# Kernel tuning notes

Measured on AMD Instinct MI355X. Metric: run time of the kernel, lower is better.

## Reference

```python
import jax, jax.numpy as jnp
import numpy as np

SMALL_CONST = 1e-8
K = 128
N = 512 * 512  # pixels


def setup_inputs() -> dict:
    key = jax.random.key(0)
    ks = jax.random.split(key, 6)
    pos = jax.random.uniform(ks[0], (N, 2), jnp.float32, 0.0, 512.0)      # pixel coords
    mu = jax.random.uniform(ks[1], (K, 2), jnp.float32, 0.0, 512.0)       # gaussian centers
    alpha = jax.random.uniform(ks[2], (K,), jnp.float32)                   # opacities in [0,1]
    color = jax.random.uniform(ks[3], (K, 3), jnp.float32, 0.0, 255.0)     # RGB in [0,255]
    scales = 10.0 + jax.random.uniform(ks[4], (K, 2), jnp.float32) * 20.0  # anisotropic scales
    thetas = jax.random.uniform(ks[5], (K,), jnp.float32, -np.pi, np.pi)   # rotations
    return dict(pos=pos, mu=mu, alpha=alpha, color=color, scales=scales, thetas=thetas)


def _forward(pos, mu, alpha, color, scales, thetas):
    # Parameter clamps done at the top of the torch forward
    alpha = jnp.clip(alpha, 0.0, 1.0)
    color = jnp.clip(color, 0.0, 255.0)
    scales = jnp.clip(scales, 0.1, None)

    # Precompute all K inverse covariances: sigma_inv = R diag(1/s^2) R^T  -> [K,2,2]
    c, s = jnp.cos(thetas), jnp.sin(thetas)
    R = jnp.stack([jnp.stack([c, -s], -1), jnp.stack([s, c], -1)], -2)  # [K,2,2]
    inv2 = 1.0 / scales ** 2                                            # [K,2]
    sigma_inv = jnp.einsum('kti,ki,kji->ktj', R, inv2, R)               # [K,2,2]

    n = pos.shape[0]
    pc0 = jnp.zeros((n, 3), pos.dtype)
    pa0 = jnp.zeros((n, 1), pos.dtype)

    def step(carry, g):
        pc, pa = carry
        mu_k, si_k, a_k, col_k = g
        diff = pos - mu_k                                          # [N,2]
        expo = -0.5 * jnp.einsum('ni,ij,nj->n', diff, si_k, diff)  # [N]
        alpha_k = (a_k * jnp.exp(expo))[:, None]                   # [N,1]
        new_alpha = pa + alpha_k * (1.0 - pa)
        pc = (pc * pa + col_k * alpha_k * (1.0 - pa)) / (new_alpha + SMALL_CONST)
        pc = jnp.clip(pc, 0.0, 255.0)
        pa = jnp.clip(new_alpha, 0.0, 1.0)
        return (pc, pa), None

    (pc, pa), _ = jax.lax.scan(jax.checkpoint(step), (pc0, pa0),
                               (mu, sigma_inv, alpha, color))
    # include_opc=True path: append alpha channel scaled to [0,255]
    return jnp.concatenate([pc, pa * 255.0], axis=-1)  # [N,4]


def reference(pos, mu, alpha, color, scales, thetas):
    return _forward(pos, mu, alpha, color, scales, thetas)
```

## Files before the change

kernel.cpp:

```cpp
#include <hip/hip_runtime.h>
#include <math.h>

#define KG 128

__global__ __launch_bounds__(256) void splat_fwd(
    const float* __restrict__ pos,
    const float* __restrict__ mu,
    const float* __restrict__ alpha,
    const float* __restrict__ color,
    const float* __restrict__ scales,
    const float* __restrict__ thetas,
    float* __restrict__ out,
    int n)
{
    __shared__ float4 sP0[KG];
    __shared__ float4 sP1[KG];
    __shared__ float  sP2[KG];

    const int tid = threadIdx.x;
    if (tid < KG) {
        const int k = tid;
        const float mx = mu[2 * k];
        const float my = mu[2 * k + 1];
        const float al = fminf(fmaxf(alpha[k], 0.0f), 1.0f);
        const float cr = fminf(fmaxf(color[3 * k + 0], 0.0f), 255.0f);
        const float cg = fminf(fmaxf(color[3 * k + 1], 0.0f), 255.0f);
        const float cb = fminf(fmaxf(color[3 * k + 2], 0.0f), 255.0f);
        const float sx = fmaxf(scales[2 * k + 0], 0.1f);
        const float sy = fmaxf(scales[2 * k + 1], 0.1f);
        const float th = thetas[k];
        const float c = cosf(th);
        const float s = sinf(th);
        const float i0 = 1.0f / (sx * sx);
        const float i1 = 1.0f / (sy * sy);
        const float a  = c * c * i0 + s * s * i1;
        const float b  = c * s * (i0 - i1);
        const float cc = s * s * i0 + c * c * i1;
        const float f = -0.5f * 1.4426950408889634f;
        sP0[k] = make_float4(mx, my, a * f, 2.0f * b * f);
        sP1[k] = make_float4(cc * f, al, cr, cg);
        sP2[k] = cb;
    }
    __syncthreads();

    const int i = blockIdx.x * blockDim.x + tid;
    if (i >= n) return;

    const float2 p = reinterpret_cast<const float2*>(pos)[i];

    float pa = 0.0f;
    float pcr = 0.0f, pcg = 0.0f, pcb = 0.0f;

#pragma unroll 4
    for (int k = 0; k < KG; ++k) {
        const float4 q0 = sP0[k];
        const float4 q1 = sP1[k];
        const float  q2 = sP2[k];
        const float dx = p.x - q0.x;
        const float dy = p.y - q0.y;
        const float e = q0.z * (dx * dx) + q0.w * (dx * dy) + q1.x * (dy * dy);
        const float w = q1.y * __builtin_amdgcn_exp2f(e);

        const float omp = 1.0f - pa;
        const float t1  = w * omp;
        const float na  = pa + t1;
        const float r   = __builtin_amdgcn_rcpf(na + 1e-8f);

        pcr = fminf(fmaxf((pcr * pa + q1.z * t1) * r, 0.0f), 255.0f);
        pcg = fminf(fmaxf((pcg * pa + q1.w * t1) * r, 0.0f), 255.0f);
        pcb = fminf(fmaxf((pcb * pa + q2  * t1) * r, 0.0f), 255.0f);
        pa  = fminf(na, 1.0f);
    }

    float4 o;
    o.x = pcr;
    o.y = pcg;
    o.z = pcb;
    o.w = pa * 255.0f;
    reinterpret_cast<float4*>(out)[i] = o;
}

extern "C" void kernel_launch(void* const* d_in, const int* in_sizes, int n_in,
                              void* d_out, int out_size, void* d_ws, size_t ws_size,
                              hipStream_t stream) {
    const float* pos    = (const float*)d_in[0];
    const float* mu     = (const float*)d_in[1];
    const float* alpha  = (const float*)d_in[2];
    const float* color  = (const float*)d_in[3];
    const float* scales = (const float*)d_in[4];
    const float* thetas = (const float*)d_in[5];
    float* out = (float*)d_out;

    const int n = in_sizes[0] / 2;
    const int block = 256;
    const int grid = (n + block - 1) / block;
    hipLaunchKernelGGL(splat_fwd, dim3(grid), dim3(block), 0, stream,
                       pos, mu, alpha, color, scales, thetas, out, n);
}
```

Measured before the change: 92.93 us.

## Process two pixels per thread with packed f32x2 math and deferred color normalization

Each thread now handles two pixels, using ext_vector float2 types so the compiler can emit packed FP32 ops (v_pk_fma/v_pk_mul). The per-step color recurrence is reformulated so it keeps an unnormalized numerator scaled by the previous reciprocal, and the clamp to [0,255] is applied only once at the end. This removes per-step clamps and shortens the dependent chain, but it changes semantics if intermediate colors would ever exceed the clamp range. It also halves the thread count, which lowers occupancy.

```diff
diff --git a/kernel.cpp b/kernel.cpp
--- a/kernel.cpp
+++ b/kernel.cpp
@@ -2,6 +2,8 @@
 #include <math.h>
 
 #define KG 128
+
+typedef float f32x2 __attribute__((ext_vector_type(2)));
 
 __global__ __launch_bounds__(256) void splat_fwd(
     const float* __restrict__ pos,
@@ -11,7 +13,7 @@
     const float* __restrict__ scales,
     const float* __restrict__ thetas,
     float* __restrict__ out,
-    int n)
+    int nPairs)
 {
     __shared__ float4 sP0[KG];
     __shared__ float4 sP1[KG];
@@ -43,41 +45,71 @@
     }
     __syncthreads();
 
-    const int i = blockIdx.x * blockDim.x + tid;
-    if (i >= n) return;
+    const int t = blockIdx.x * blockDim.x + tid;
+    if (t >= nPairs) return;
 
-    const float2 p = reinterpret_cast<const float2*>(pos)[i];
+    const float4 pp = reinterpret_cast<const float4*>(pos)[t];
+    const f32x2 px = { pp.x, pp.z };
+    const f32x2 py = { pp.y, pp.w };
 
-    float pa = 0.0f;
-    float pcr = 0.0f, pcg = 0.0f, pcb = 0.0f;
+    f32x2 pa    = { 0.0f, 0.0f };
+    f32x2 rprev = { 0.0f, 0.0f };
+    f32x2 numr  = { 0.0f, 0.0f };
+    f32x2 numg  = { 0.0f, 0.0f };
+    f32x2 numb  = { 0.0f, 0.0f };
 
 #pragma unroll 4
     for (int k = 0; k < KG; ++k) {
         const float4 q0 = sP0[k];
         const float4 q1 = sP1[k];
         const float  q2 = sP2[k];
-        const float dx = p.x - q0.x;
-        const float dy = p.y - q0.y;
-        const float e = q0.z * (dx * dx) + q0.w * (dx * dy) + q1.x * (dy * dy);
-        const float w = q1.y * __builtin_amdgcn_exp2f(e);
 
-        const float omp = 1.0f - pa;
-        const float t1  = w * omp;
-        const float na  = pa + t1;
-        const float r   = __builtin_amdgcn_rcpf(na + 1e-8f);
+        const f32x2 dx = px - q0.x;
+        const f32x2 dy = py - q0.y;
+        const f32x2 u  = q0.z * dx + q0.w * dy;
+        const f32x2 e  = dx * u + (q1.x * dy) * dy;
 
-        pcr = fminf(fmaxf((pcr * pa + q1.z * t1) * r, 0.0f), 255.0f);
-        pcg = fminf(fmaxf((pcg * pa + q1.w * t1) * r, 0.0f), 255.0f);
-        pcb = fminf(fmaxf((pcb * pa + q2  * t1) * r, 0.0f), 255.0f);
-        pa  = fminf(na, 1.0f);
+        f32x2 E;
+        E.x = __builtin_amdgcn_exp2f(e.x);
+        E.y = __builtin_amdgcn_exp2f(e.y);
+
+        const f32x2 w   = q1.y * E;
+        const f32x2 omp = 1.0f - pa;
+        const f32x2 t1  = w * omp;
+        const f32x2 na  = pa + t1;
+        const f32x2 nae = na + 1e-8f;
+
+        f32x2 r;
+        r.x = __builtin_amdgcn_rcpf(nae.x);
+        r.y = __builtin_amdgcn_rcpf(nae.y);
+
+        const f32x2 h = rprev * pa;
+        numr = numr * h + q1.z * t1;
+        numg = numg * h + q1.w * t1;
+        numb = numb * h + q2  * t1;
+
+        pa.x = fminf(na.x, 1.0f);
+        pa.y = fminf(na.y, 1.0f);
+        rprev = r;
     }
 
-    float4 o;
-    o.x = pcr;
-    o.y = pcg;
-    o.z = pcb;
-    o.w = pa * 255.0f;
-    reinterpret_cast<float4*>(out)[i] = o;
+    const f32x2 pcr = numr * rprev;
+    const f32x2 pcg = numg * rprev;
+    const f32x2 pcb = numb * rprev;
+
+    float4 o0, o1;
+    o0.x = fminf(fmaxf(pcr.x, 0.0f), 255.0f);
+    o0.y = fminf(fmaxf(pcg.x, 0.0f), 255.0f);
+    o0.z = fminf(fmaxf(pcb.x, 0.0f), 255.0f);
+    o0.w = pa.x * 255.0f;
+    o1.x = fminf(fmaxf(pcr.y, 0.0f), 255.0f);
+    o1.y = fminf(fmaxf(pcg.y, 0.0f), 255.0f);
+    o1.z = fminf(fmaxf(pcb.y, 0.0f), 255.0f);
+    o1.w = pa.y * 255.0f;
+
+    float4* o = reinterpret_cast<float4*>(out);
+    o[2 * t]     = o0;
+    o[2 * t + 1] = o1;
 }
 
 extern "C" void kernel_launch(void* const* d_in, const int* in_sizes, int n_in,
@@ -92,8 +124,9 @@
     float* out = (float*)d_out;
 
     const int n = in_sizes[0] / 2;
+    const int nPairs = n / 2;
     const int block = 256;
-    const int grid = (n + block - 1) / block;
+    const int grid = (nPairs + block - 1) / block;
     hipLaunchKernelGGL(splat_fwd, dim3(grid), dim3(block), 0, stream,
-                       pos, mu, alpha, color, scales, thetas, out, n);
+                       pos, mu, alpha, color, scales, thetas, out, nPairs);
 }
```

Result: faster. 81.55 us (-12.2%).
